# Performance work log

Hardware: AMD Instinct MI355X
Metric: run time of the kernel (lower is better)

## Reference

```python
import jax, jax.numpy as jnp
import numpy as np

N, E, IN_FEATS, H = 20000, 320000, 512, 64
EPS = 1e-5  # BatchNorm eps


def setup_inputs() -> dict:
    key = jax.random.key(0)
    ks = iter(jax.random.split(key, 64))
    rn = lambda *s: jax.random.normal(next(ks), s, dtype=jnp.float32)
    d = {}
    d["x"] = rn(N, IN_FEATS)
    d["edge_index"] = jax.random.randint(next(ks), (2, E), 0, N)
    d["Wm"] = rn(IN_FEATS, H) * 0.05; d["bm"] = rn(H) * 0.05
    d["Wc"] = rn(IN_FEATS, H) * 0.05; d["bc"] = rn(H) * 0.05
    d["Wg1"] = rn(H, 2 * H) * 0.05;     d["bg1"] = rn(2 * H) * 0.05
    d["Wg2"] = rn(2 * H, 2 * H) * 0.05; d["bg2"] = rn(2 * H) * 0.05
    d["Wg3"] = rn(2 * H, 4 * H) * 0.05; d["bg3"] = rn(4 * H) * 0.05
    for name, cin in (("e1", 8 * H), ("e2", 4 * H), ("e3", 4 * H)):
        d[name + "_gamma"] = 1.0 + rn(cin) * 0.1
        d[name + "_beta"] = rn(cin) * 0.1
        d[name + "_mean"] = rn(cin) * 0.1
        d[name + "_var"] = jax.random.uniform(next(ks), (cin,), dtype=jnp.float32) + 0.5
        d[name + "_W"] = rn(cin, 2 * H) * 0.05
    d["Wfc"] = rn(2 * H, 1) * 0.05; d["bfc"] = rn(1) * 0.05
    return d


def _gcn(x, W, b, src, dst, n):
    """PyG GCNConv: self-loops + symmetric normalization + sum aggregation."""
    h = x @ W  # [N, out]
    loop = jnp.arange(n)
    s = jnp.concatenate([src, loop])
    d = jnp.concatenate([dst, loop])
    deg = jax.ops.segment_sum(jnp.ones(s.shape[0], h.dtype), d, num_segments=n)
    dinv = jnp.where(deg > 0, jax.lax.rsqrt(deg), 0.0)
    msg = h[s] * (dinv[s] * dinv[d])[:, None]  # gather + normalize
    return jax.ops.segment_sum(msg, d, num_segments=n) + b


def _edge_conv(x, gamma, beta, mean, var, W, src, dst, n):
    """PyG EdgeConv with LinearPathPreact nn (BN->ReLU->Linear), max aggregation."""
    xi = x[dst]
    xj = x[src]
    feat = jnp.concatenate([xi, xj - xi], axis=-1)  # [E, 2*C]
    h = (feat - mean) * jax.lax.rsqrt(var + EPS) * gamma + beta  # BN (eval stats)
    h = jnp.maximum(h, 0.0) @ W  # ReLU -> Linear(bias=False)
    out = jax.ops.segment_max(h, dst, num_segments=n)
    return jnp.where(jnp.isfinite(out), out, 0.0)  # empty segments -> 0


def reference(x, edge_index, Wm, bm, Wc, bc, Wg1, bg1, Wg2, bg2, Wg3, bg3,
              e1_gamma, e1_beta, e1_mean, e1_var, e1_W,
              e2_gamma, e2_beta, e2_mean, e2_var, e2_W,
              e3_gamma, e3_beta, e3_mean, e3_var, e3_W,
              Wfc, bfc):
    n = x.shape[0]
    src, dst = edge_index[0], edge_index[1]
    x0_main = x @ Wm + bm
    x0 = x @ Wc + bc
    x0 = x0.at[0::4].set(x0_main[0::4])  # main-person rows use the main projection
    g = _gcn(x0, Wg1, bg1, src, dst, n)
    g = _gcn(g, Wg2, bg2, src, dst, n)
    g = _gcn(g, Wg3, bg3, src, dst, n)
    h = _edge_conv(g, e1_gamma, e1_beta, e1_mean, e1_var, e1_W, src, dst, n)
    h = _edge_conv(h, e2_gamma, e2_beta, e2_mean, e2_var, e2_W, src, dst, n)
    h = _edge_conv(h, e3_gamma, e3_beta, e3_mean, e3_var, e3_W, src, dst, n)
    return h @ Wfc + bfc  # [N, 1]
```

## Files before the change

### kernel.cpp

```cpp
#include <hip/hip_runtime.h>

#define DEVINL __device__ __forceinline__

constexpr int N_NODES  = 20000;
constexpr int N_EDGES  = 320000;
constexpr int IN_FEATS = 512;

static_assert(N_EDGES % 64 == 0, "edge tiling assumes E % 64 == 0");
static_assert(N_NODES % 16 == 0, "proj assumes N % 16 == 0");

typedef __attribute__((ext_vector_type(8))) short short8;
typedef __attribute__((ext_vector_type(4))) float f32x4;

DEVINL unsigned enc_f32(float v) {
  unsigned b = __float_as_uint(v);
  return (b & 0x80000000u) ? ~b : (b | 0x80000000u);
}
DEVINL float dec_f32(unsigned e) {
  unsigned b = (e & 0x80000000u) ? (e & 0x7FFFFFFFu) : ~e;
  return __uint_as_float(b);
}
DEVINL float dech(unsigned q, float p) { return q ? (p + dec_f32(q)) : 0.f; }

DEVINL unsigned short bf16_rne(float f) {
  unsigned u = __float_as_uint(f);
  u += 0x7FFFu + ((u >> 16) & 1u);
  return (unsigned short)(u >> 16);
}
DEVINL void split_bf16(float v, unsigned short& h, unsigned short& l) {
  h = bf16_rne(v);
  float hf = __uint_as_float((unsigned)h << 16);
  l = bf16_rne(v - hf);
}

DEVINL void glds16(const unsigned short* g, unsigned short* l) {
  __builtin_amdgcn_global_load_lds(
      (const __attribute__((address_space(1))) unsigned int*)g,
      (__attribute__((address_space(3))) unsigned int*)l, 16, 0, 0);
}

__global__ void hist_kernel(const int* __restrict__ dst, int* __restrict__ cnt, int e) {
  int i = blockIdx.x * 256 + threadIdx.x;
  if (i < e) atomicAdd(&cnt[dst[i]], 1);
}
__global__ void __launch_bounds__(256)
scan_p1(const int* __restrict__ cnt, int* __restrict__ rp, int* __restrict__ bsum,
        float* __restrict__ dinv, float* __restrict__ dinv2, int n) {
  __shared__ int buf[256];
  int i = blockIdx.x * 256 + threadIdx.x;
  int v = (i < n) ? cnt[i] : 0;
  if (i < n) {
    float s = rsqrtf((float)v + 1.0f);
    dinv[i] = s;
    dinv2[i] = s * s;
  }
  buf[threadIdx.x] = v;
  __syncthreads();
  for (int off = 1; off < 256; off <<= 1) {
    int t = (threadIdx.x >= off) ? buf[threadIdx.x - off] : 0;
    __syncthreads();
    buf[threadIdx.x] += t;
    __syncthreads();
  }
  if (i < n) rp[i] = buf[threadIdx.x] - v;
  if (threadIdx.x == 255) bsum[blockIdx.x] = buf[255];
}
__global__ void __launch_bounds__(256)
scan_p2(int* __restrict__ bsum, int nb) {
  __shared__ int buf[256];
  int v = (threadIdx.x < nb) ? bsum[threadIdx.x] : 0;
  buf[threadIdx.x] = v;
  __syncthreads();
  for (int off = 1; off < 256; off <<= 1) {
    int t = (threadIdx.x >= off) ? buf[threadIdx.x - off] : 0;
    __syncthreads();
    buf[threadIdx.x] += t;
    __syncthreads();
  }
  if (threadIdx.x < nb) bsum[threadIdx.x] = buf[threadIdx.x] - v;
}
__global__ void __launch_bounds__(256)
scan_p3(int* __restrict__ rp, const int* __restrict__ bsum, int* __restrict__ cursor,
        int n, int e) {
  int i = blockIdx.x * 256 + threadIdx.x;
  if (i < n) {
    int v = rp[i] + bsum[blockIdx.x];
    rp[i] = v;
    cursor[i] = v;
  }
  if (i == 0) rp[n] = e;
}
__global__ void scatter_edges_kernel(const int* __restrict__ src, const int* __restrict__ dst,
                                     int* __restrict__ cursor, int* __restrict__ ssrc,
                                     int* __restrict__ sdst, int e) {
  int i = blockIdx.x * 256 + threadIdx.x;
  if (i < e) {
    int d = dst[i];
    int pos = atomicAdd(&cursor[d], 1);
    ssrc[pos] = src[i];
    sdst[pos] = d;
  }
}

__global__ void uvec1_kernel(const int* __restrict__ row_ptr, const int* __restrict__ ssrc,
                             const float* __restrict__ dinv, float* __restrict__ u1,
                             float* __restrict__ w1, int n) {
  int d = blockIdx.x * 256 + threadIdx.x;
  if (d >= n) return;
  float s = dinv[d];
  float acc = s;
  int e = row_ptr[d], end = row_ptr[d + 1];
  for (; e < end; ++e) acc += dinv[ssrc[e]];
  float u = s * acc;
  u1[d] = u;
  w1[d] = s * u;
}
__global__ void uvec2_kernel(const int* __restrict__ row_ptr, const int* __restrict__ ssrc,
                             const float* __restrict__ dinv, const float* __restrict__ w1,
                             float* __restrict__ u2, int n) {
  int d = blockIdx.x * 256 + threadIdx.x;
  if (d >= n) return;
  float acc = w1[d];
  int e = row_ptr[d], end = row_ptr[d + 1];
  for (; e < end; ++e) acc += w1[ssrc[e]];
  u2[d] = dinv[d] * acc;
}

__global__ void smallmm2(const float* __restrict__ A1, const float* __restrict__ B1,
                         float* __restrict__ C1, int m1, int k1, int n1,
                         const float* __restrict__ A2, const float* __restrict__ B2,
                         float* __restrict__ C2, int m2, int k2, int n2) {
  int i = blockIdx.x * 256 + threadIdx.x;
  int t1 = m1 * n1;
  if (i < t1) {
    int r = i / n1, c = i % n1;
    float acc = 0.f;
    for (int kk = 0; kk < k1; ++kk) acc = fmaf(A1[r * k1 + kk], B1[kk * n1 + c], acc);
    C1[i] = acc;
  } else {
    i -= t1;
    if (i < m2 * n2) {
      int r = i / n2, c = i % n2;
      float acc = 0.f;
      for (int kk = 0; kk < k2; ++kk) acc = fmaf(A2[r * k2 + kk], B2[kk * n2 + c], acc);
      C2[i] = acc;
    }
  }
}

DEVINL void bn1(const float* g, const float* b, const float* m, const float* v,
                float* sc, float* sh, int i) {
  float s = g[i] * rsqrtf(v[i] + 1e-5f);
  sc[i] = s;
  sh[i] = b[i] - m[i] * s;
}
DEVINL void wfrag1(const float* W, unsigned short* out, int e) {
  int k = e >> 7, c = e & 127;
  unsigned short h, l;
  split_bf16(W[e], h, l);
  int chunk = k >> 5, kq = (k >> 3) & 3, j = k & 7, ct = c >> 4, n = c & 15;
  int frag = (ct * 4 + kq) * 16 + n;
  size_t o = (size_t)chunk * 8192 + frag * 8 + j;
  out[o] = h;
  out[o + 4096] = l;
}
__global__ void setup_kernel(const float* __restrict__ e1W, const float* __restrict__ e2W,
                             const float* __restrict__ e3W, unsigned short* b1p,
                             unsigned short* b1q, unsigned short* b2p, unsigned short* b2q,
                             unsigned short* b3p, unsigned short* b3q,
                             const float* g1, const float* b1, const float* m1,
                             const float* v1, float* sc1, float* sh1, const float* g2,
                             const float* b2, const float* m2, const float* v2, float* sc2,
                             float* sh2, const float* g3, const float* b3, const float* m3,
                             const float* v3, float* sc3, float* sh3) {
  if (blockIdx.x < 512) {
    int g = blockIdx.x * 256 + threadIdx.x;
    if (g < 32768) wfrag1(e1W, b1p, g);
    else if (g < 65536) wfrag1(e1W + 32768, b1q, g - 32768);
    else if (g < 81920) wfrag1(e2W, b2p, g - 65536);
    else if (g < 98304) wfrag1(e2W + 16384, b2q, g - 81920);
    else if (g < 114688) wfrag1(e3W, b3p, g - 98304);
    else wfrag1(e3W + 16384, b3q, g - 114688);
  } else {
    for (int i = threadIdx.x; i < 1024; i += 256) {
      if (i < 512) bn1(g1, b1, m1, v1, sc1, sh1, i);
      else if (i < 768) bn1(g2, b2, m2, v2, sc2, sh2, i - 512);
      else bn1(g3, b3, m3, v3, sc3, sh3, i - 768);
    }
  }
}

__global__ void combine_kernel(unsigned* __restrict__ Q, const float* __restrict__ P,
                               float* __restrict__ H, int n) {
  int i = blockIdx.x * 256 + threadIdx.x;
  if (i < n) {
    unsigned e = Q[i];
    H[i] = dech(e, P[i]);
    Q[i] = 0u;
  }
}

__global__ void __launch_bounds__(256)
proj_kernel(const float* __restrict__ X, const float* __restrict__ Wm,
            const float* __restrict__ bm, const float* __restrict__ Wc,
            const float* __restrict__ bc, const float* __restrict__ dinv,
            float* __restrict__ Y0) {
  __shared__ float xs[16][IN_FEATS];
  int tid = threadIdx.x;
  int rowBase = blockIdx.x * 16;
  for (int i = 0; i < 8; ++i) {
    int idx = i * 256 + tid;
    int r = idx >> 7, kq = idx & 127;
    *reinterpret_cast<float4*>(&xs[r][kq * 4]) =
        *reinterpret_cast<const float4*>(X + (size_t)(rowBase + r) * IN_FEATS + kq * 4);
  }
  __syncthreads();
  int r4 = tid >> 6;
  int j = tid & 63;
  const float* W = (r4 == 0) ? Wm : Wc;
  float a0 = 0.f, a1 = 0.f, a2 = 0.f, a3 = 0.f;
#pragma unroll 4
  for (int k = 0; k < IN_FEATS; ++k) {
    float w = W[k * 64 + j];
    a0 = fmaf(xs[r4][k], w, a0);
    a1 = fmaf(xs[r4 + 4][k], w, a1);
    a2 = fmaf(xs[r4 + 8][k], w, a2);
    a3 = fmaf(xs[r4 + 12][k], w, a3);
  }
  float b = (r4 == 0) ? bm[j] : bc[j];
  int r0 = rowBase + r4;
  Y0[(size_t)r0 * 64 + j] = (a0 + b) * dinv[r0];
  Y0[(size_t)(r0 + 4) * 64 + j] = (a1 + b) * dinv[r0 + 4];
  Y0[(size_t)(r0 + 8) * 64 + j] = (a2 + b) * dinv[r0 + 8];
  Y0[(size_t)(r0 + 12) * 64 + j] = (a3 + b) * dinv[r0 + 12];
}

template <int LOGF4>
__global__ void __launch_bounds__(256)
agg_kernel(const float* __restrict__ Y, const int* __restrict__ row_ptr,
           const int* __restrict__ ssrc, const float* __restrict__ mfac,
           float* __restrict__ Z, int n) {
  constexpr int F4 = 1 << LOGF4;
  int g = blockIdx.x * 256 + threadIdx.x;
  int d = g >> LOGF4, c4 = g & (F4 - 1);
  if (d >= n) return;
  const float4* Yp = (const float4*)Y;
  float4 a = Yp[(size_t)d * F4 + c4];
  float ax = a.x, ay = a.y, az = a.z, aw = a.w;
  int e = row_ptr[d], end = row_ptr[d + 1];
  for (; e + 7 < end; e += 8) {
    int s[8];
#pragma unroll
    for (int i = 0; i < 8; ++i) s[i] = ssrc[e + i];
    float4 v[8];
#pragma unroll
    for (int i = 0; i < 8; ++i) v[i] = Yp[(size_t)s[i] * F4 + c4];
#pragma unroll
    for (int i = 0; i < 8; ++i) {
      ax += v[i].x; ay += v[i].y; az += v[i].z; aw += v[i].w;
    }
  }
  for (; e < end; ++e) {
    float4 v = Yp[(size_t)ssrc[e] * F4 + c4];
    ax += v.x; ay += v.y; az += v.z; aw += v.w;
  }
  float s = mfac[d];
  ((float4*)Z)[(size_t)d * F4 + c4] = make_float4(ax * s, ay * s, az * s, aw * s);
}

__global__ void __launch_bounds__(256)
gemm_rank1_kernel(const float* __restrict__ X, const float* __restrict__ W,
                  const float* __restrict__ b3, const float* __restrict__ u1,
                  const float* __restrict__ u2, const float* __restrict__ c1,
                  const float* __restrict__ c2, float* __restrict__ H, int n) {
  constexpr int K = 64, F = 256;
  __shared__ float Xs[64][K + 1];
  __shared__ float Ws[K][65];
  int tid = threadIdx.x;
  int rowBase = blockIdx.x * 64;
  int colBase = blockIdx.y * 64;
  for (int idx = tid; idx < 64 * K; idx += 256) {
    int r = idx / K, k = idx % K;
    int row = rowBase + r;
    Xs[r][k] = (row < n) ? X[(size_t)row * K + k] : 0.f;
  }
  for (int idx = tid; idx < K * 64; idx += 256) {
    int k = idx >> 6, c = idx & 63;
    Ws[k][c] = W[(size_t)k * F + colBase + c];
  }
  __syncthreads();
  int tx = tid & 15, ty = tid >> 4;
  float acc[4][4] = {};
  for (int k = 0; k < K; ++k) {
    float a[4], b[4];
#pragma unroll
    for (int r = 0; r < 4; ++r) a[r] = Xs[ty * 4 + r][k];
#pragma unroll
    for (int c = 0; c < 4; ++c) b[c] = Ws[k][tx * 4 + c];
#pragma unroll
    for (int r = 0; r < 4; ++r)
#pragma unroll
      for (int c = 0; c < 4; ++c) acc[r][c] = fmaf(a[r], b[c], acc[r][c]);
  }
#pragma unroll
  for (int r = 0; r < 4; ++r) {
    int row = rowBase + ty * 4 + r;
    if (row < n) {
      float du2 = u2[row], du1 = u1[row];
#pragma unroll
      for (int c = 0; c < 4; ++c) {
        int col = colBase + tx * 4 + c;
        float v = acc[r][c] + du2 * c1[col] + du1 * c2[col] + b3[col];
        H[(size_t)row * F + col] = v;
      }
    }
  }
}

DEVINL void proc8(const float4& va, const float4& vb, const float4& sa, const float4& sb,
                  const float4& ha, const float4& hb, short8& hi, short8& lo) {
  float f[8] = {va.x, va.y, va.z, va.w, vb.x, vb.y, vb.z, vb.w};
  float s[8] = {sa.x, sa.y, sa.z, sa.w, sb.x, sb.y, sb.z, sb.w};
  float t[8] = {ha.x, ha.y, ha.z, ha.w, hb.x, hb.y, hb.z, hb.w};
#pragma unroll
  for (int j = 0; j < 8; ++j) {
    float v = fmaxf(fmaf(f[j], s[j], t[j]), 0.f);
    unsigned short hh, ll;
    split_bf16(v, hh, ll);
    hi[j] = (short)hh;
    lo[j] = (short)ll;
  }
}

template <int C>
__global__ void __launch_bounds__(256, 4)
ec_mfma_kernel(const float* __restrict__ X, const int* __restrict__ ssrc,
               const int* __restrict__ sdst,
               const float* __restrict__ scaleQ, const float* __restrict__ shiftQ,
               const unsigned short* __restrict__ BfragQ,
               const float* __restrict__ scaleP, const float* __restrict__ shiftP,
               const unsigned short* __restrict__ BfragP,
               unsigned* __restrict__ outU, float* __restrict__ outP,
               int nrows, int edge_blocks) {
  constexpr int NCH = C / 32;
  constexpr int NSTAGE = NCH / 2;
  __shared__ unsigned short Bmat[16384];
  __shared__ float ss[2 * C];
  __shared__ int de_s[64];
  const int tid = threadIdx.x, lane = tid & 63, wv = tid >> 6;
  const int q = lane >> 4, mn = lane & 15;
  const bool EDGE = (int)blockIdx.x < edge_blocks;
  const int base = (EDGE ? (int)blockIdx.x : (int)blockIdx.x - edge_blocks) * 64;
  const int koff = q * 8;
  const int lr = wv * 16 + mn;

  const float* scale = EDGE ? scaleQ : scaleP;
  const float* shift = EDGE ? shiftQ : shiftP;
  const unsigned short* Bfrag = EDGE ? BfragQ : BfragP;

  int id, is = 0;
  if (EDGE) {
    if (tid < 64) de_s[tid] = sdst[base + tid];
    is = ssrc[base + lr];
    id = sdst[base + lr];
  } else {
    id = min(base + lr, nrows - 1);
  }
  const float* pd = X + (size_t)id * C + koff;
  const float* ps = EDGE ? X + (size_t)is * C + koff : nullptr;

  f32x4 acc[8];
#pragma unroll
  for (int i = 0; i < 8; ++i) acc[i] = (f32x4)0.f;

  float4 A[2][4];
#define LOAD_A(cc, slot)                              \
  {                                                   \
    const int kk_ = (cc) * 32;                        \
    A[slot][0] = *(const float4*)(pd + kk_);          \
    A[slot][1] = *(const float4*)(pd + kk_ + 4);      \
    if (EDGE) {                                       \
      A[slot][2] = *(const float4*)(ps + kk_);        \
      A[slot][3] = *(const float4*)(ps + kk_ + 4);    \
    }                                                 \
  }

  LOAD_A(0, 0);
  {
    constexpr int NF4 = C / 4;
    if (tid < NF4)
      ((float4*)ss)[tid] = ((const float4*)scale)[tid];
    else if (tid < 2 * NF4)
      ((float4*)(ss + C))[tid - NF4] = ((const float4*)shift)[tid - NF4];
  }
  {
    const unsigned short* bs = Bfrag + lane * 8;
#pragma unroll
    for (int i = 0; i < 8; ++i) {
      int seg = wv * 8 + i;
      glds16(bs + seg * 512, Bmat + seg * 512);
    }
  }

#pragma unroll
  for (int s = 0; s < NSTAGE; ++s) {
    if (s > 0) {
      __syncthreads();
      const unsigned short* bs = Bfrag + (size_t)s * 16384 + lane * 8;
#pragma unroll
      for (int i = 0; i < 8; ++i) {
        int seg = wv * 8 + i;
        glds16(bs + seg * 512, Bmat + seg * 512);
      }
    }
    __syncthreads();
#pragma unroll
    for (int cc = 0; cc < 2; ++cc) {
      const int c = s * 2 + cc;
      const int kc = c * 32;
      if (c + 1 < NCH) LOAD_A(c + 1, (c + 1) & 1);
      float4 sca = *(const float4*)&ss[kc + koff];
      float4 scb = *(const float4*)&ss[kc + koff + 4];
      float4 sha = *(const float4*)&ss[C + kc + koff];
      float4 shb = *(const float4*)&ss[C + kc + koff + 4];
      const int sl = c & 1;
      float4 u0, u1;
      if (EDGE) {
        u0 = make_float4(A[sl][2].x - A[sl][0].x, A[sl][2].y - A[sl][0].y,
                         A[sl][2].z - A[sl][0].z, A[sl][2].w - A[sl][0].w);
        u1 = make_float4(A[sl][3].x - A[sl][1].x, A[sl][3].y - A[sl][1].y,
                         A[sl][3].z - A[sl][1].z, A[sl][3].w - A[sl][1].w);
      } else {
        u0 = A[sl][0];
        u1 = A[sl][1];
      }
      short8 ah, al;
      proc8(u0, u1, sca, scb, sha, shb, ah, al);
      const unsigned short* Bc = Bmat + cc * 8192;
#pragma unroll
      for (int ct = 0; ct < 8; ++ct) {
        int fi = ct * 64 + lane;
        short8 bh = *(const short8*)(Bc + fi * 8);
        short8 bl = *(const short8*)(Bc + 4096 + fi * 8);
        acc[ct] = __builtin_amdgcn_mfma_f32_16x16x32_bf16(ah, bh, acc[ct], 0, 0, 0);
        acc[ct] = __builtin_amdgcn_mfma_f32_16x16x32_bf16(ah, bl, acc[ct], 0, 0, 0);
        acc[ct] = __builtin_amdgcn_mfma_f32_16x16x32_bf16(al, bh, acc[ct], 0, 0, 0);
      }
    }
  }
#undef LOAD_A

  if (EDGE) {
    int e0 = wv * 16 + q * 4;
#pragma unroll
    for (int ct = 0; ct < 8; ++ct) {
      int f = ct * 16 + mn;
      int prev = de_s[e0];
      float mv = acc[ct][0];
#pragma unroll
      for (int r = 1; r < 4; ++r) {
        int d = de_s[e0 + r];
        float v = acc[ct][r];
        if (d == prev) {
          mv = fmaxf(mv, v);
        } else {
          atomicMax(&outU[(size_t)prev * 128 + f], enc_f32(mv));
          prev = d;
          mv = v;
        }
      }
      atomicMax(&outU[(size_t)prev * 128 + f], enc_f32(mv));
    }
  } else {
    int r0 = base + wv * 16 + q * 4;
#pragma unroll
    for (int ct = 0; ct < 8; ++ct) {
      int f = ct * 16 + mn;
#pragma unroll
      for (int r = 0; r < 4; ++r) {
        int row = r0 + r;
        if (row < nrows) outP[(size_t)row * 128 + f] = acc[ct][r];
      }
    }
  }
}

__global__ void __launch_bounds__(256)
fc_kernel(const unsigned* __restrict__ Q, const float* __restrict__ P,
          const float* __restrict__ Wfc, const float* __restrict__ bfc,
          float* __restrict__ out, int n) {
  int g = blockIdx.x * 256 + threadIdx.x;
  int node = g >> 6, lane = g & 63;
  if (node >= n) return;
  size_t b = (size_t)node * 128;
  float h0 = dech(Q[b + lane], P[b + lane]);
  float h1 = dech(Q[b + 64 + lane], P[b + 64 + lane]);
  float v = fmaf(h0, Wfc[lane], h1 * Wfc[64 + lane]);
#pragma unroll
  for (int off = 32; off > 0; off >>= 1) v += __shfl_down(v, off);
  if (lane == 0) out[node] = v + bfc[0];
}

extern "C" void kernel_launch(void* const* d_in, const int* in_sizes, int n_in,
                              void* d_out, int out_size, void* d_ws, size_t ws_size,
                              hipStream_t stream) {
  const float* x   = (const float*)d_in[0];
  const int*   ei  = (const int*)d_in[1];
  const float* Wm  = (const float*)d_in[2];
  const float* bm  = (const float*)d_in[3];
  const float* Wc  = (const float*)d_in[4];
  const float* bc  = (const float*)d_in[5];
  const float* Wg1 = (const float*)d_in[6];
  const float* bg1 = (const float*)d_in[7];
  const float* Wg2 = (const float*)d_in[8];
  const float* bg2 = (const float*)d_in[9];
  const float* Wg3 = (const float*)d_in[10];
  const float* bg3 = (const float*)d_in[11];
  const float* e1g = (const float*)d_in[12];
  const float* e1b = (const float*)d_in[13];
  const float* e1m = (const float*)d_in[14];
  const float* e1v = (const float*)d_in[15];
  const float* e1W = (const float*)d_in[16];
  const float* e2g = (const float*)d_in[17];
  const float* e2b = (const float*)d_in[18];
  const float* e2m = (const float*)d_in[19];
  const float* e2v = (const float*)d_in[20];
  const float* e2W = (const float*)d_in[21];
  const float* e3g = (const float*)d_in[22];
  const float* e3b = (const float*)d_in[23];
  const float* e3m = (const float*)d_in[24];
  const float* e3v = (const float*)d_in[25];
  const float* e3W = (const float*)d_in[26];
  const float* Wfc = (const float*)d_in[27];
  const float* bfc = (const float*)d_in[28];

  const int* src = ei;
  const int* dst = ei + N_EDGES;

  float* ws    = (float*)d_ws;
  float* dinv  = ws;
  float* dinv2 = dinv + N_NODES;
  float* u1    = dinv2 + N_NODES;
  float* w1    = u1 + N_NODES;
  float* u2    = w1 + N_NODES;
  float* y0    = u2 + N_NODES;
  float* za    = y0 + (size_t)N_NODES * 64;
  float* zb    = za + (size_t)N_NODES * 64;
  float* PQ    = zb + (size_t)N_NODES * 64;
  float* G     = PQ + (size_t)N_NODES * 256;
  float* sc1   = G + (size_t)N_NODES * 256;
  float* sh1   = sc1 + 512;
  float* sc2   = sh1 + 512;
  float* sh2   = sc2 + 256;
  float* sc3   = sh2 + 256;
  float* sh3   = sc3 + 256;
  unsigned short* bf1p = (unsigned short*)(sh3 + 256);
  unsigned short* bf1q = bf1p + 65536;
  unsigned short* bf2p = bf1q + 65536;
  unsigned short* bf2q = bf2p + 32768;
  unsigned short* bf3p = bf2q + 32768;
  unsigned short* bf3q = bf3p + 32768;
  float* W23   = (float*)(bf3q + 32768);
  float* W123  = W23 + 32768;
  float* c1    = W123 + 16384;
  float* c2    = c1 + 256;
  int* cnt     = (int*)(c2 + 256);
  int* row_ptr = cnt + N_NODES;
  int* cursor  = row_ptr + N_NODES + 1;
  int* bsum    = cursor + N_NODES;
  int* ssrc    = bsum + 256;
  int* sdst    = ssrc + N_EDGES;

  float*    Pbuf = PQ;
  unsigned* Qbuf = (unsigned*)(PQ + (size_t)N_NODES * 128);

  hipMemsetAsync(cnt, 0, N_NODES * sizeof(int), stream);
  hist_kernel<<<N_EDGES / 256, 256, 0, stream>>>(dst, cnt, N_EDGES);
  scan_p1<<<79, 256, 0, stream>>>(cnt, row_ptr, bsum, dinv, dinv2, N_NODES);
  scan_p2<<<1, 256, 0, stream>>>(bsum, 79);
  scan_p3<<<79, 256, 0, stream>>>(row_ptr, bsum, cursor, N_NODES, N_EDGES);
  scatter_edges_kernel<<<N_EDGES / 256, 256, 0, stream>>>(src, dst, cursor, ssrc, sdst,
                                                          N_EDGES);

  smallmm2<<<129, 256, 0, stream>>>(Wg2, Wg3, W23, 128, 128, 256,
                                    bg2, Wg3, c2, 1, 128, 256);
  smallmm2<<<65, 256, 0, stream>>>(Wg1, W23, W123, 64, 128, 256,
                                   bg1, W23, c1, 1, 128, 256);
  uvec1_kernel<<<79, 256, 0, stream>>>(row_ptr, ssrc, dinv, u1, w1, N_NODES);
  uvec2_kernel<<<79, 256, 0, stream>>>(row_ptr, ssrc, dinv, w1, u2, N_NODES);

  setup_kernel<<<513, 256, 0, stream>>>(e1W, e2W, e3W, bf1p, bf1q, bf2p, bf2q, bf3p, bf3q,
                                        e1g, e1b, e1m, e1v, sc1, sh1, e2g, e2b, e2m, e2v,
                                        sc2, sh2, e3g, e3b, e3m, e3v, sc3, sh3);

  proj_kernel<<<N_NODES / 16, 256, 0, stream>>>(x, Wm, bm, Wc, bc, dinv, y0);
  agg_kernel<4><<<N_NODES * 16 / 256, 256, 0, stream>>>(y0, row_ptr, ssrc, dinv2, za, N_NODES);
  agg_kernel<4><<<N_NODES * 16 / 256, 256, 0, stream>>>(za, row_ptr, ssrc, dinv2, zb, N_NODES);
  agg_kernel<4><<<N_NODES * 16 / 256, 256, 0, stream>>>(zb, row_ptr, ssrc, dinv, za, N_NODES);
  dim3 grid4(313, 4);
  gemm_rank1_kernel<<<grid4, 256, 0, stream>>>(za, W123, bg3, u1, u2, c1, c2, G, N_NODES);

  const int EDGE_BLOCKS = N_EDGES / 64;
  const int NODE_BLOCKS = (N_NODES + 63) / 64;
  const int EC_BLOCKS   = EDGE_BLOCKS + NODE_BLOCKS;
  const int NB_ELEM     = N_NODES * 128 / 256;

  float* H1 = G;
  float* H2 = G + (size_t)N_NODES * 128;

  hipMemsetAsync(Qbuf, 0, (size_t)N_NODES * 128 * 4, stream);
  ec_mfma_kernel<256><<<EC_BLOCKS, 256, 0, stream>>>(
      G, ssrc, sdst, sc1 + 256, sh1 + 256, bf1q, sc1, sh1, bf1p, Qbuf, Pbuf, N_NODES,
      EDGE_BLOCKS);
  combine_kernel<<<NB_ELEM, 256, 0, stream>>>(Qbuf, Pbuf, H1, N_NODES * 128);

  ec_mfma_kernel<128><<<EC_BLOCKS, 256, 0, stream>>>(
      H1, ssrc, sdst, sc2 + 128, sh2 + 128, bf2q, sc2, sh2, bf2p, Qbuf, Pbuf, N_NODES,
      EDGE_BLOCKS);
  combine_kernel<<<NB_ELEM, 256, 0, stream>>>(Qbuf, Pbuf, H2, N_NODES * 128);

  ec_mfma_kernel<128><<<EC_BLOCKS, 256, 0, stream>>>(
      H2, ssrc, sdst, sc3 + 128, sh3 + 128, bf3q, sc3, sh3, bf3p, Qbuf, Pbuf, N_NODES,
      EDGE_BLOCKS);
  fc_kernel<<<N_NODES * 64 / 256, 256, 0, stream>>>(Qbuf, Pbuf, Wfc, bfc, (float*)d_out,
                                                    N_NODES);
}
```

Before: 704.9 us.

## Fuse setup launches, fold Q zeroing into setup, halve EdgeConv LDS stage

Merges the small weight-product kernels, the first u-vector pass and the Q-buffer memset into fewer launches. setup_kernel now also computes Wg1·Wg2, bg1·Wg2 and zeroes Qbuf, and a new mid_kernel computes W123, c1, c2 and u1/w1. The EdgeConv MFMA kernel stages one 32-wide K chunk of B in LDS per step instead of two, halving shared memory and raising the occupancy hint from 4 to 8 blocks. The cost is more __syncthreads and B reloads per block, and register pressure under the tighter launch bound.

```diff
diff --git a/kernel.cpp b/kernel.cpp
--- a/kernel.cpp
+++ b/kernel.cpp
@@ -102,18 +102,102 @@
   }
 }
 
-__global__ void uvec1_kernel(const int* __restrict__ row_ptr, const int* __restrict__ ssrc,
-                             const float* __restrict__ dinv, float* __restrict__ u1,
-                             float* __restrict__ w1, int n) {
-  int d = blockIdx.x * 256 + threadIdx.x;
-  if (d >= n) return;
-  float s = dinv[d];
-  float acc = s;
-  int e = row_ptr[d], end = row_ptr[d + 1];
-  for (; e < end; ++e) acc += dinv[ssrc[e]];
-  float u = s * acc;
-  u1[d] = u;
-  w1[d] = s * u;
+DEVINL void bn1(const float* g, const float* b, const float* m, const float* v,
+                float* sc, float* sh, int i) {
+  float s = g[i] * rsqrtf(v[i] + 1e-5f);
+  sc[i] = s;
+  sh[i] = b[i] - m[i] * s;
+}
+DEVINL void wfrag1(const float* W, unsigned short* out, int e) {
+  int k = e >> 7, c = e & 127;
+  unsigned short h, l;
+  split_bf16(W[e], h, l);
+  int chunk = k >> 5, kq = (k >> 3) & 3, j = k & 7, ct = c >> 4, n = c & 15;
+  int frag = (ct * 4 + kq) * 16 + n;
+  size_t o = (size_t)chunk * 8192 + frag * 8 + j;
+  out[o] = h;
+  out[o + 4096] = l;
+}
+__global__ void setup_kernel(const float* __restrict__ e1W, const float* __restrict__ e2W,
+                             const float* __restrict__ e3W, unsigned short* b1p,
+                             unsigned short* b1q, unsigned short* b2p, unsigned short* b2q,
+                             unsigned short* b3p, unsigned short* b3q,
+                             const float* g1, const float* b1, const float* m1,
+                             const float* v1bn, float* sc1, float* sh1, const float* g2,
+                             const float* b2, const float* m2, const float* v2, float* sc2,
+                             float* sh2, const float* g3, const float* b3, const float* m3,
+                             const float* v3, float* sc3, float* sh3,
+                             const float* __restrict__ Wg1, const float* __restrict__ Wg2,
+                             const float* __restrict__ bg1, float* __restrict__ W12,
+                             float* __restrict__ v1out, unsigned* __restrict__ Qzero) {
+  int bid = blockIdx.x;
+  if (bid < 512) {
+    int g = bid * 256 + threadIdx.x;
+    if (g < 32768) wfrag1(e1W, b1p, g);
+    else if (g < 65536) wfrag1(e1W + 32768, b1q, g - 32768);
+    else if (g < 81920) wfrag1(e2W, b2p, g - 65536);
+    else if (g < 98304) wfrag1(e2W + 16384, b2q, g - 81920);
+    else if (g < 114688) wfrag1(e3W, b3p, g - 98304);
+    else wfrag1(e3W + 16384, b3q, g - 114688);
+  } else if (bid == 512) {
+    for (int i = threadIdx.x; i < 1024; i += 256) {
+      if (i < 512) bn1(g1, b1, m1, v1bn, sc1, sh1, i);
+      else if (i < 768) bn1(g2, b2, m2, v2, sc2, sh2, i - 512);
+      else bn1(g3, b3, m3, v3, sc3, sh3, i - 768);
+    }
+  } else if (bid < 545) {
+    int i = (bid - 513) * 256 + threadIdx.x;
+    int r = i >> 7, c = i & 127;
+    float acc = 0.f;
+    for (int k = 0; k < 128; ++k) acc = fmaf(Wg1[r * 128 + k], Wg2[k * 128 + c], acc);
+    W12[i] = acc;
+  } else if (bid == 545) {
+    if (threadIdx.x < 128) {
+      int c = threadIdx.x;
+      float acc = 0.f;
+      for (int k = 0; k < 128; ++k) acc = fmaf(bg1[k], Wg2[k * 128 + c], acc);
+      v1out[c] = acc;
+    }
+  } else {
+    int i = (bid - 546) * 256 + threadIdx.x;
+    ((uint4*)Qzero)[i] = make_uint4(0u, 0u, 0u, 0u);
+  }
+}
+
+__global__ void mid_kernel(const float* __restrict__ W12, const float* __restrict__ Wg3,
+                           const float* __restrict__ v1, const float* __restrict__ bg2,
+                           float* __restrict__ W123, float* __restrict__ c1,
+                           float* __restrict__ c2, const int* __restrict__ row_ptr,
+                           const int* __restrict__ ssrc, const float* __restrict__ dinv,
+                           float* __restrict__ u1, float* __restrict__ w1, int n) {
+  int bid = blockIdx.x;
+  if (bid < 64) {
+    int i = bid * 256 + threadIdx.x;
+    int r = i >> 8, c = i & 255;
+    float acc = 0.f;
+    for (int k = 0; k < 128; ++k) acc = fmaf(W12[r * 128 + k], Wg3[k * 256 + c], acc);
+    W123[i] = acc;
+  } else if (bid == 64) {
+    int c = threadIdx.x;
+    float acc = 0.f;
+    for (int k = 0; k < 128; ++k) acc = fmaf(v1[k], Wg3[k * 256 + c], acc);
+    c1[c] = acc;
+  } else if (bid == 65) {
+    int c = threadIdx.x;
+    float acc = 0.f;
+    for (int k = 0; k < 128; ++k) acc = fmaf(bg2[k], Wg3[k * 256 + c], acc);
+    c2[c] = acc;
+  } else {
+    int d = (bid - 66) * 256 + threadIdx.x;
+    if (d >= n) return;
+    float s = dinv[d];
+    float acc = s;
+    int e = row_ptr[d], end = row_ptr[d + 1];
+    for (; e < end; ++e) acc += dinv[ssrc[e]];
+    float u = s * acc;
+    u1[d] = u;
+    w1[d] = s * u;
+  }
 }
 __global__ void uvec2_kernel(const int* __restrict__ row_ptr, const int* __restrict__ ssrc,
                              const float* __restrict__ dinv, const float* __restrict__ w1,
@@ -124,70 +208,6 @@
   int e = row_ptr[d], end = row_ptr[d + 1];
   for (; e < end; ++e) acc += w1[ssrc[e]];
   u2[d] = dinv[d] * acc;
-}
-
-__global__ void smallmm2(const float* __restrict__ A1, const float* __restrict__ B1,
-                         float* __restrict__ C1, int m1, int k1, int n1,
-                         const float* __restrict__ A2, const float* __restrict__ B2,
-                         float* __restrict__ C2, int m2, int k2, int n2) {
-  int i = blockIdx.x * 256 + threadIdx.x;
-  int t1 = m1 * n1;
-  if (i < t1) {
-    int r = i / n1, c = i % n1;
-    float acc = 0.f;
-    for (int kk = 0; kk < k1; ++kk) acc = fmaf(A1[r * k1 + kk], B1[kk * n1 + c], acc);
-    C1[i] = acc;
-  } else {
-    i -= t1;
-    if (i < m2 * n2) {
-      int r = i / n2, c = i % n2;
-      float acc = 0.f;
-      for (int kk = 0; kk < k2; ++kk) acc = fmaf(A2[r * k2 + kk], B2[kk * n2 + c], acc);
-      C2[i] = acc;
-    }
-  }
-}
-
-DEVINL void bn1(const float* g, const float* b, const float* m, const float* v,
-                float* sc, float* sh, int i) {
-  float s = g[i] * rsqrtf(v[i] + 1e-5f);
-  sc[i] = s;
-  sh[i] = b[i] - m[i] * s;
-}
-DEVINL void wfrag1(const float* W, unsigned short* out, int e) {
-  int k = e >> 7, c = e & 127;
-  unsigned short h, l;
-  split_bf16(W[e], h, l);
-  int chunk = k >> 5, kq = (k >> 3) & 3, j = k & 7, ct = c >> 4, n = c & 15;
-  int frag = (ct * 4 + kq) * 16 + n;
-  size_t o = (size_t)chunk * 8192 + frag * 8 + j;
-  out[o] = h;
-  out[o + 4096] = l;
-}
-__global__ void setup_kernel(const float* __restrict__ e1W, const float* __restrict__ e2W,
-                             const float* __restrict__ e3W, unsigned short* b1p,
-                             unsigned short* b1q, unsigned short* b2p, unsigned short* b2q,
-                             unsigned short* b3p, unsigned short* b3q,
-                             const float* g1, const float* b1, const float* m1,
-                             const float* v1, float* sc1, float* sh1, const float* g2,
-                             const float* b2, const float* m2, const float* v2, float* sc2,
-                             float* sh2, const float* g3, const float* b3, const float* m3,
-                             const float* v3, float* sc3, float* sh3) {
-  if (blockIdx.x < 512) {
-    int g = blockIdx.x * 256 + threadIdx.x;
-    if (g < 32768) wfrag1(e1W, b1p, g);
-    else if (g < 65536) wfrag1(e1W + 32768, b1q, g - 32768);
-    else if (g < 81920) wfrag1(e2W, b2p, g - 65536);
-    else if (g < 98304) wfrag1(e2W + 16384, b2q, g - 81920);
-    else if (g < 114688) wfrag1(e3W, b3p, g - 98304);
-    else wfrag1(e3W + 16384, b3q, g - 114688);
-  } else {
-    for (int i = threadIdx.x; i < 1024; i += 256) {
-      if (i < 512) bn1(g1, b1, m1, v1, sc1, sh1, i);
-      else if (i < 768) bn1(g2, b2, m2, v2, sc2, sh2, i - 512);
-      else bn1(g3, b3, m3, v3, sc3, sh3, i - 768);
-    }
-  }
 }
 
 __global__ void combine_kernel(unsigned* __restrict__ Q, const float* __restrict__ P,
@@ -333,7 +353,7 @@
 }
 
 template <int C>
-__global__ void __launch_bounds__(256, 4)
+__global__ void __launch_bounds__(256, 8)
 ec_mfma_kernel(const float* __restrict__ X, const int* __restrict__ ssrc,
                const int* __restrict__ sdst,
                const float* __restrict__ scaleQ, const float* __restrict__ shiftQ,
@@ -343,8 +363,7 @@
                unsigned* __restrict__ outU, float* __restrict__ outP,
                int nrows, int edge_blocks) {
   constexpr int NCH = C / 32;
-  constexpr int NSTAGE = NCH / 2;
-  __shared__ unsigned short Bmat[16384];
+  __shared__ unsigned short Bmat[8192];
   __shared__ float ss[2 * C];
   __shared__ int de_s[64];
   const int tid = threadIdx.x, lane = tid & 63, wv = tid >> 6;
@@ -396,56 +415,51 @@
   {
     const unsigned short* bs = Bfrag + lane * 8;
 #pragma unroll
-    for (int i = 0; i < 8; ++i) {
-      int seg = wv * 8 + i;
+    for (int i = 0; i < 4; ++i) {
+      int seg = wv * 4 + i;
       glds16(bs + seg * 512, Bmat + seg * 512);
     }
   }
 
 #pragma unroll
-  for (int s = 0; s < NSTAGE; ++s) {
-    if (s > 0) {
+  for (int c = 0; c < NCH; ++c) {
+    if (c > 0) {
       __syncthreads();
-      const unsigned short* bs = Bfrag + (size_t)s * 16384 + lane * 8;
-#pragma unroll
-      for (int i = 0; i < 8; ++i) {
-        int seg = wv * 8 + i;
+      const unsigned short* bs = Bfrag + (size_t)c * 8192 + lane * 8;
+#pragma unroll
+      for (int i = 0; i < 4; ++i) {
+        int seg = wv * 4 + i;
         glds16(bs + seg * 512, Bmat + seg * 512);
       }
     }
     __syncthreads();
-#pragma unroll
-    for (int cc = 0; cc < 2; ++cc) {
-      const int c = s * 2 + cc;
-      const int kc = c * 32;
-      if (c + 1 < NCH) LOAD_A(c + 1, (c + 1) & 1);
-      float4 sca = *(const float4*)&ss[kc + koff];
-      float4 scb = *(const float4*)&ss[kc + koff + 4];
-      float4 sha = *(const float4*)&ss[C + kc + koff];
-      float4 shb = *(const float4*)&ss[C + kc + koff + 4];
-      const int sl = c & 1;
-      float4 u0, u1;
-      if (EDGE) {
-        u0 = make_float4(A[sl][2].x - A[sl][0].x, A[sl][2].y - A[sl][0].y,
-                         A[sl][2].z - A[sl][0].z, A[sl][2].w - A[sl][0].w);
-        u1 = make_float4(A[sl][3].x - A[sl][1].x, A[sl][3].y - A[sl][1].y,
-                         A[sl][3].z - A[sl][1].z, A[sl][3].w - A[sl][1].w);
-      } else {
-        u0 = A[sl][0];
-        u1 = A[sl][1];
-      }
-      short8 ah, al;
-      proc8(u0, u1, sca, scb, sha, shb, ah, al);
-      const unsigned short* Bc = Bmat + cc * 8192;
-#pragma unroll
-      for (int ct = 0; ct < 8; ++ct) {
-        int fi = ct * 64 + lane;
-        short8 bh = *(const short8*)(Bc + fi * 8);
-        short8 bl = *(const short8*)(Bc + 4096 + fi * 8);
-        acc[ct] = __builtin_amdgcn_mfma_f32_16x16x32_bf16(ah, bh, acc[ct], 0, 0, 0);
-        acc[ct] = __builtin_amdgcn_mfma_f32_16x16x32_bf16(ah, bl, acc[ct], 0, 0, 0);
-        acc[ct] = __builtin_amdgcn_mfma_f32_16x16x32_bf16(al, bh, acc[ct], 0, 0, 0);
-      }
+    const int kc = c * 32;
+    if (c + 1 < NCH) LOAD_A(c + 1, (c + 1) & 1);
+    float4 sca = *(const float4*)&ss[kc + koff];
+    float4 scb = *(const float4*)&ss[kc + koff + 4];
+    float4 sha = *(const float4*)&ss[C + kc + koff];
+    float4 shb = *(const float4*)&ss[C + kc + koff + 4];
+    const int sl = c & 1;
+    float4 u0, u1;
+    if (EDGE) {
+      u0 = make_float4(A[sl][2].x - A[sl][0].x, A[sl][2].y - A[sl][0].y,
+                       A[sl][2].z - A[sl][0].z, A[sl][2].w - A[sl][0].w);
+      u1 = make_float4(A[sl][3].x - A[sl][1].x, A[sl][3].y - A[sl][1].y,
+                       A[sl][3].z - A[sl][1].z, A[sl][3].w - A[sl][1].w);
+    } else {
+      u0 = A[sl][0];
+      u1 = A[sl][1];
+    }
+    short8 ah, al;
+    proc8(u0, u1, sca, scb, sha, shb, ah, al);
+#pragma unroll
+    for (int ct = 0; ct < 8; ++ct) {
+      int fi = ct * 64 + lane;
+      short8 bh = *(const short8*)(Bmat + fi * 8);
+      short8 bl = *(const short8*)(Bmat + 4096 + fi * 8);
+      acc[ct] = __builtin_amdgcn_mfma_f32_16x16x32_bf16(ah, bh, acc[ct], 0, 0, 0);
+      acc[ct] = __builtin_amdgcn_mfma_f32_16x16x32_bf16(ah, bl, acc[ct], 0, 0, 0);
+      acc[ct] = __builtin_amdgcn_mfma_f32_16x16x32_bf16(al, bh, acc[ct], 0, 0, 0);
     }
   }
 #undef LOAD_A
@@ -560,8 +574,9 @@
   unsigned short* bf2q = bf2p + 32768;
   unsigned short* bf3p = bf2q + 32768;
   unsigned short* bf3q = bf3p + 32768;
-  float* W23   = (float*)(bf3q + 32768);
-  float* W123  = W23 + 32768;
+  float* W12   = (float*)(bf3q + 32768);
+  float* v1    = W12 + 8192;
+  float* W123  = v1 + 128;
   float* c1    = W123 + 16384;
   float* c2    = c1 + 256;
   int* cnt     = (int*)(c2 + 256);
@@ -582,16 +597,14 @@
   scatter_edges_kernel<<<N_EDGES / 256, 256, 0, stream>>>(src, dst, cursor, ssrc, sdst,
                                                           N_EDGES);
 
-  smallmm2<<<129, 256, 0, stream>>>(Wg2, Wg3, W23, 128, 128, 256,
-                                    bg2, Wg3, c2, 1, 128, 256);
-  smallmm2<<<65, 256, 0, stream>>>(Wg1, W23, W123, 64, 128, 256,
-                                   bg1, W23, c1, 1, 128, 256);
-  uvec1_kernel<<<79, 256, 0, stream>>>(row_ptr, ssrc, dinv, u1, w1, N_NODES);
+  setup_kernel<<<3046, 256, 0, stream>>>(e1W, e2W, e3W, bf1p, bf1q, bf2p, bf2q, bf3p, bf3q,
+                                         e1g, e1b, e1m, e1v, sc1, sh1, e2g, e2b, e2m, e2v,
+                                         sc2, sh2, e3g, e3b, e3m, e3v, sc3, sh3,
+                                         Wg1, Wg2, bg1, W12, v1, Qbuf);
+
+  mid_kernel<<<145, 256, 0, stream>>>(W12, Wg3, v1, bg2, W123, c1, c2, row_ptr, ssrc, dinv,
+                                      u1, w1, N_NODES);
   uvec2_kernel<<<79, 256, 0, stream>>>(row_ptr, ssrc, dinv, w1, u2, N_NODES);
-
-  setup_kernel<<<513, 256, 0, stream>>>(e1W, e2W, e3W, bf1p, bf1q, bf2p, bf2q, bf3p, bf3q,
-                                        e1g, e1b, e1m, e1v, sc1, sh1, e2g, e2b, e2m, e2v,
-                                        sc2, sh2, e3g, e3b, e3m, e3v, sc3, sh3);
 
   proj_kernel<<<N_NODES / 16, 256, 0, stream>>>(x, Wm, bm, Wc, bc, dinv, y0);
   agg_kernel<4><<<N_NODES * 16 / 256, 256, 0, stream>>>(y0, row_ptr, ssrc, dinv2, za, N_NODES);
@@ -608,7 +621,6 @@
   float* H1 = G;
   float* H2 = G + (size_t)N_NODES * 128;
 
-  hipMemsetAsync(Qbuf, 0, (size_t)N_NODES * 128 * 4, stream);
   ec_mfma_kernel<256><<<EC_BLOCKS, 256, 0, stream>>>(
       G, ssrc, sdst, sc1 + 256, sh1 + 256, bf1q, sc1, sh1, bf1p, Qbuf, Pbuf, N_NODES,
       EDGE_BLOCKS);
```

Result: slower. 1.093 ms (+55.1%).
